# Optimization experiments

Measured on AMD Instinct MI355X. Metric: run time of the kernel, lower is better.

The kernel has to match this reference:

```python
import jax, jax.numpy as jnp
import numpy as np


def setup_inputs() -> dict:
    key = jax.random.key(0)
    k1, k2, k3 = jax.random.split(key, 3)
    b, n, h, d = 2, 2048, 16, 64
    q = jax.random.normal(k1, (b, n, h, d), dtype=jnp.float32)
    k = jax.random.normal(k2, (b, n, h, d), dtype=jnp.float32)
    v = jax.random.normal(k3, (b, n, h, d), dtype=jnp.float32)
    return {"q": q, "k": k, "v": v, "is_causal": 1}


def reference(q, k, v, is_causal):
    # q, k, v: [b, n, h, d] -> attention computed in [b, h, n, d] layout
    b, n, h, d = q.shape
    scale = 1.0 / jnp.sqrt(jnp.asarray(d, dtype=q.dtype))
    # scores: [b, h, n_q, n_k]
    scores = jnp.einsum("bqhd,bkhd->bhqk", q, k) * scale
    if is_causal:
        causal_mask = jnp.triu(jnp.ones((n, n), dtype=bool), k=1)  # True above diag
        scores = jnp.where(causal_mask[None, None], -jnp.inf, scores)
    attn = jax.nn.softmax(scores, axis=-1)
    out = jnp.einsum("bhqk,bkhd->bqhd", attn, v)  # back to [b, n, h, d]
    return out
```

## Files before the change

### kernel.cpp

```cpp
#include <hip/hip_runtime.h>
#include <hip/hip_bf16.h>

namespace {

constexpr int Nn = 2048;
constexpr int Hh = 16;
constexpr int Dd = 64;
constexpr int ROWSTR = Hh * Dd;
constexpr int KVB = 64;
constexpr int NTILES = Nn / KVB;
constexpr size_t IMG_TILE = 16384;
constexpr size_t WS_NEED = (size_t)32 * NTILES * IMG_TILE;

typedef __bf16 bf16x8 __attribute__((ext_vector_type(8)));
typedef __bf16 bf16x4 __attribute__((ext_vector_type(4)));
typedef float  f32x16 __attribute__((ext_vector_type(16)));

__global__ __launch_bounds__(256, 2) void prep_kernel(
    const float* __restrict__ Kg, const float* __restrict__ Vg,
    char* __restrict__ ws) {
  const int bid = blockIdx.x;
  const int bh  = bid & 31;
  const int T   = bid >> 5;
  const int tid = threadIdx.x;
  const int b = bh >> 4, h = bh & 15;
  const size_t base = ((size_t)b * Nn * Hh + h) * Dd;
  const float* kp = Kg + base;
  const float* vp = Vg + base;
  char* img = ws + (size_t)(bh * NTILES + T) * IMG_TILE;

  {
    const int row = tid >> 2;
    const int seg = tid & 3;
    const float* kr = kp + (size_t)(T * 64 + row) * ROWSTR + seg * 16;
    float4 f0 = ((const float4*)kr)[0];
    float4 f1 = ((const float4*)kr)[1];
    float4 f2 = ((const float4*)kr)[2];
    float4 f3 = ((const float4*)kr)[3];
    const int half = row >> 5, l31r = row & 31;
    char* slotp = img + (half * 4 + seg) * 1024;
    bf16x8 w0 = { (__bf16)f0.x, (__bf16)f0.y, (__bf16)f0.z, (__bf16)f0.w,
                  (__bf16)f1.x, (__bf16)f1.y, (__bf16)f1.z, (__bf16)f1.w };
    bf16x8 w1 = { (__bf16)f2.x, (__bf16)f2.y, (__bf16)f2.z, (__bf16)f2.w,
                  (__bf16)f3.x, (__bf16)f3.y, (__bf16)f3.z, (__bf16)f3.w };
    *(bf16x8*)(slotp + l31r * 16) = w0;
    *(bf16x8*)(slotp + (l31r + 32) * 16) = w1;
  }
  char* imgV = img + 8192;
#pragma unroll
  for (int e2 = 0; e2 < 2; ++e2) {
    const int e = e2 * 256 + tid;
    const int slotV = e >> 6, lane = e & 63;
    const int kc = slotV >> 1, df = slotV & 1;
    const int l31e = lane & 31, g2e = lane >> 5;
    const int d = 32 * df + l31e;
    const size_t kv0 = (size_t)(T * 64 + 16 * kc + 4 * g2e);
    const float* vb = vp + d;
    bf16x8 w;
#pragma unroll
    for (int i2 = 0; i2 < 4; ++i2) w[i2]     = (__bf16)vb[(kv0 + i2) * ROWSTR];
#pragma unroll
    for (int i2 = 0; i2 < 4; ++i2) w[4 + i2] = (__bf16)vb[(kv0 + 8 + i2) * ROWSTR];
    *(bf16x8*)(imgV + slotV * 1024 + lane * 16) = w;
  }
}

__global__ __launch_bounds__(256, 2) void fattn_kernel(
    const float* __restrict__ Qg, const char* __restrict__ ws,
    const int* __restrict__ flag, float* __restrict__ Og) {
  __shared__ __align__(16) char smem[2][2][16384];

  const int tid  = threadIdx.x;
  const int lane = tid & 63;
  const int wv   = tid >> 6;
  const int grp  = wv >> 1;
  const int st   = wv & 1;
  const int l31  = lane & 31;
  const int g2   = lane >> 5;

  const int bid = blockIdx.x;
  const int bh  = ((bid & 7) << 2) | ((bid >> 3) & 3);
  const int j   = bid >> 5;
  const int b   = bh >> 4;
  const int h   = bh & 15;
  const int causal = flag[0];

  const size_t base = ((size_t)b * Nn * Hh + h) * Dd;
  const float* qp = Qg + base;
  const char*  img = ws + (size_t)bh * NTILES * IMG_TILE;
  float*       op = Og + base;

  const float SCALE = 0.125f * 1.44269504088896340736f;

  for (int pass = 0; pass < 2; ++pass) {
    const int Tq = pass ? j : (31 - j);
    const int qs = Tq * 64 + st * 32;
    const int NI = causal ? ((Tq + 2) >> 1) : (NTILES / 2);
    const int nC = causal ? ((Tq >= grp) ? (((Tq - grp) >> 1) + 1) : 0)
                          : (NTILES / 2);

    __syncthreads();

    bf16x8 qf[4];
#pragma unroll
    for (int dc = 0; dc < 4; ++dc) {
      const float* qrow = qp + (size_t)(qs + l31) * ROWSTR + dc * 16 + g2 * 8;
      float4 a = *(const float4*)qrow;
      float4 c = *(const float4*)(qrow + 4);
      qf[dc][0] = (__bf16)(a.x * SCALE); qf[dc][1] = (__bf16)(a.y * SCALE);
      qf[dc][2] = (__bf16)(a.z * SCALE); qf[dc][3] = (__bf16)(a.w * SCALE);
      qf[dc][4] = (__bf16)(c.x * SCALE); qf[dc][5] = (__bf16)(c.y * SCALE);
      qf[dc][6] = (__bf16)(c.z * SCALE); qf[dc][7] = (__bf16)(c.w * SCALE);
    }

    f32x16 acc0 = {};
    f32x16 acc1 = {};
    float m_run = -INFINITY;
    float l_run = 0.0f;

    {
      bf16x8 stg[8];
#pragma unroll
      for (int it = 0; it < 8; ++it)
        stg[it] = *(const bf16x8*)(img + (it * 256 + tid) * 16);
#pragma unroll
      for (int it = 0; it < 8; ++it)
        *(bf16x8*)(&smem[0][it >> 2][0] + ((it & 3) * 256 + tid) * 16) = stg[it];
    }

    for (int i = 0; i < NI; ++i) {
      __syncthreads();
      const bool pf = (i + 1 < NI);
      bf16x8 stg[8];
      if (pf) {
        const char* src = img + (size_t)(2 * i + 2) * IMG_TILE;
#pragma unroll
        for (int it = 0; it < 8; ++it)
          stg[it] = *(const bf16x8*)(src + (it * 256 + tid) * 16);
      }

      if (i < nC) {
        const char* kb = &smem[i & 1][grp][0];
        const char* vb = kb + 8192;

        f32x16 s0 = {}, s1 = {};
        __builtin_amdgcn_s_setprio(1);
#pragma unroll
        for (int dc = 0; dc < 4; ++dc) {
          bf16x8 kf0 = *(const bf16x8*)(kb + (dc)     * 1024 + lane * 16);
          bf16x8 kf1 = *(const bf16x8*)(kb + (4 + dc) * 1024 + lane * 16);
          s0 = __builtin_amdgcn_mfma_f32_32x32x16_bf16(kf0, qf[dc], s0, 0, 0, 0);
          s1 = __builtin_amdgcn_mfma_f32_32x32x16_bf16(kf1, qf[dc], s1, 0, 0, 0);
        }
        __builtin_amdgcn_s_setprio(0);

        if (causal && (2 * i + grp) == Tq) {
          const int kvb = Tq * KVB;
          const int qrow = qs + l31;
#pragma unroll
          for (int rr = 0; rr < 16; ++rr) {
            int rm = (rr & 3) + ((rr >> 2) << 3) + (g2 << 2);
            if (kvb + rm > qrow)      s0[rr] = -INFINITY;
            if (kvb + 32 + rm > qrow) s1[rr] = -INFINITY;
          }
        }

        float p8[8];
#pragma unroll
        for (int e = 0; e < 8; ++e)
          p8[e] = fmaxf(fmaxf(s0[e], s0[e + 8]), fmaxf(s1[e], s1[e + 8]));
        float mt = fmaxf(fmaxf(fmaxf(p8[0], p8[1]), fmaxf(p8[2], p8[3])),
                         fmaxf(fmaxf(p8[4], p8[5]), fmaxf(p8[6], p8[7])));
        mt = fmaxf(mt, __shfl_xor(mt, 32));
        const float mnew = fmaxf(m_run, mt);

#pragma unroll
        for (int rr = 0; rr < 16; ++rr) {
          s0[rr] = __builtin_amdgcn_exp2f(s0[rr] - mnew);
          s1[rr] = __builtin_amdgcn_exp2f(s1[rr] - mnew);
        }
        float q8[8];
#pragma unroll
        for (int e = 0; e < 8; ++e)
          q8[e] = (s0[e] + s0[e + 8]) + (s1[e] + s1[e + 8]);
        float rs = ((q8[0] + q8[1]) + (q8[2] + q8[3])) +
                   ((q8[4] + q8[5]) + (q8[6] + q8[7]));
        rs += __shfl_xor(rs, 32);
        if (__all(mt <= m_run)) {
          l_run += rs;
        } else {
          const float alpha = __builtin_amdgcn_exp2f(m_run - mnew);
#pragma unroll
          for (int rr = 0; rr < 16; ++rr) {
            float at = __shfl(alpha, (rr & 3) + ((rr >> 2) << 3) + (g2 << 2));
            acc0[rr] *= at;
            acc1[rr] *= at;
          }
          l_run = l_run * alpha + rs;
          m_run = mnew;
        }

        bf16x8 pa[4];
#pragma unroll
        for (int kc = 0; kc < 4; ++kc) {
          const f32x16& sv = (kc < 2) ? s0 : s1;
          const int rbase = (kc & 1) * 8;
#pragma unroll
          for (int jj = 0; jj < 8; ++jj) pa[kc][jj] = (__bf16)sv[rbase + jj];
        }

        __builtin_amdgcn_s_setprio(1);
#pragma unroll
        for (int kc = 0; kc < 4; ++kc) {
#pragma unroll
          for (int df = 0; df < 2; ++df) {
            bf16x8 vf = *(const bf16x8*)(vb + (kc * 2 + df) * 1024 + lane * 16);
            if (df == 0)
              acc0 = __builtin_amdgcn_mfma_f32_32x32x16_bf16(pa[kc], vf, acc0, 0, 0, 0);
            else
              acc1 = __builtin_amdgcn_mfma_f32_32x32x16_bf16(pa[kc], vf, acc1, 0, 0, 0);
          }
        }
        __builtin_amdgcn_s_setprio(0);
      }

      if (pf) {
#pragma unroll
        for (int it = 0; it < 8; ++it)
          *(bf16x8*)(&smem[(i + 1) & 1][it >> 2][0] +
                     ((it & 3) * 256 + tid) * 16) = stg[it];
      }
    }

    __syncthreads();
    float* arena = (float*)&smem[0][0][0];
    if (grp == 1) {
      float* ab = arena + st * 2112;
#pragma unroll
      for (int rr = 0; rr < 16; ++rr) {
        int rm = (rr & 3) + ((rr >> 2) << 3) + (g2 << 2);
        ab[rm * 64 + l31]      = acc0[rr];
        ab[rm * 64 + 32 + l31] = acc1[rr];
      }
      if (g2 == 0) { ab[2048 + l31] = m_run; ab[2080 + l31] = l_run; }
    }
    __syncthreads();
    if (grp == 0) {
      const float* ab = arena + st * 2112;
      const float mB = ab[2048 + l31];
      const float lB = ab[2080 + l31];
      const float mN = fmaxf(m_run, mB);
      float fA = __builtin_amdgcn_exp2f(m_run - mN);
      float fB = __builtin_amdgcn_exp2f(mB - mN);
      const float lT = l_run * fA + lB * fB;
      const float linv = 1.0f / lT;
      fA *= linv; fB *= linv;
#pragma unroll
      for (int rr = 0; rr < 16; ++rr) {
        const int rm = (rr & 3) + ((rr >> 2) << 3) + (g2 << 2);
        const float FA = __shfl(fA, rm);
        const float FB = __shfl(fB, rm);
        const float o0 = acc0[rr] * FA + ab[rm * 64 + l31] * FB;
        const float o1 = acc1[rr] * FA + ab[rm * 64 + 32 + l31] * FB;
        const size_t row = (size_t)(qs + rm) * ROWSTR;
        op[row + l31]      = o0;
        op[row + 32 + l31] = o1;
      }
    }
  }
}

__device__ __forceinline__ int swzK(int row, int colByte) {
  return (row * 128 + colByte) ^ ((row & 7) << 4);
}
__device__ __forceinline__ int swzV(int row, int colByte) {
  return (row * 128 + colByte) ^ (((row & 7) << 4) | (((row >> 3) & 1) << 3));
}
struct SR { float4 k[4]; float v[16]; };
__device__ __forceinline__ void fb_issue(const float* kp, const float* vp,
                                         int kv0, int tid, SR& s) {
#pragma unroll
  for (int it = 0; it < 4; ++it) {
    int idx = it * 256 + tid;
    int kvr = idx >> 4, c4 = idx & 15;
    s.k[it] = *(const float4*)(kp + (size_t)(kv0 + kvr) * ROWSTR + c4 * 4);
  }
#pragma unroll
  for (int it = 0; it < 4; ++it) {
    int idx = it * 256 + tid;
    int d8 = idx & 63, kv4 = idx >> 6;
#pragma unroll
    for (int i2 = 0; i2 < 4; ++i2)
      s.v[it * 4 + i2] = vp[(size_t)(kv0 + kv4 * 4 + i2) * ROWSTR + d8];
  }
}
__device__ __forceinline__ void fb_write(char* kb, char* vb, int tid, const SR& s) {
#pragma unroll
  for (int it = 0; it < 4; ++it) {
    int idx = it * 256 + tid;
    int kvr = idx >> 4, c4 = idx & 15;
    bf16x4 w = { (__bf16)s.k[it].x, (__bf16)s.k[it].y,
                 (__bf16)s.k[it].z, (__bf16)s.k[it].w };
    *(bf16x4*)(kb + swzK(kvr, c4 * 8)) = w;
  }
#pragma unroll
  for (int it = 0; it < 4; ++it) {
    int idx = it * 256 + tid;
    int d8 = idx & 63, kv4 = idx >> 6;
    bf16x4 w = { (__bf16)s.v[it * 4 + 0], (__bf16)s.v[it * 4 + 1],
                 (__bf16)s.v[it * 4 + 2], (__bf16)s.v[it * 4 + 3] };
    *(bf16x4*)(vb + swzV(d8, kv4 * 8)) = w;
  }
}
__global__ __launch_bounds__(256, 2) void fattn_fb(
    const float* __restrict__ Qg, const float* __restrict__ Kg,
    const float* __restrict__ Vg, const int* __restrict__ flag,
    float* __restrict__ Og) {
  __shared__ __align__(16) char smem[16384];
  const int tid  = threadIdx.x;
  const int lane = tid & 63;
  const int wv   = tid >> 6;
  const int l31  = lane & 31;
  const int g2   = lane >> 5;
  const int bid = blockIdx.x;
  const int pidx = bid >> 1;
  const int side = bid & 1;
  const int bh  = ((pidx & 7) << 2) | (pidx >> 6);
  const int ti  = (pidx >> 3) & 7;
  const int b   = bh >> 4;
  const int h   = bh & 15;
  const int causal = flag[0];
  const int Tq  = side ? ti : (15 - ti);
  const size_t base = ((size_t)b * Nn * Hh + h) * Dd;
  const float* qp = Qg + base;
  const float* kp = Kg + base;
  const float* vp = Vg + base;
  float*       op = Og + base;
  const float SCALE = 0.125f * 1.44269504088896340736f;
  const int qs = Tq * 128 + wv * 32;
  const int Tblock = causal ? (2 * Tq + 2) : NTILES;
  const int Twave  = causal ? ((qs + 31) / KVB + 1) : NTILES;
  bf16x8 qf[4];
#pragma unroll
  for (int dc = 0; dc < 4; ++dc) {
    const float* qrow = qp + (size_t)(qs + l31) * ROWSTR + dc * 16 + g2 * 8;
    float4 a = *(const float4*)qrow;
    float4 c = *(const float4*)(qrow + 4);
    qf[dc][0] = (__bf16)(a.x * SCALE); qf[dc][1] = (__bf16)(a.y * SCALE);
    qf[dc][2] = (__bf16)(a.z * SCALE); qf[dc][3] = (__bf16)(a.w * SCALE);
    qf[dc][4] = (__bf16)(c.x * SCALE); qf[dc][5] = (__bf16)(c.y * SCALE);
    qf[dc][6] = (__bf16)(c.z * SCALE); qf[dc][7] = (__bf16)(c.w * SCALE);
  }
  f32x16 acc0 = {}, acc1 = {};
  float m_run = -INFINITY, l_run = 0.0f;
  SR st;
  fb_issue(kp, vp, 0, tid, st);
  fb_write(smem, smem + 8192, tid, st);
  for (int t = 0; t < Tblock; ++t) {
    __syncthreads();
    const bool pf = (t + 1 < Tblock);
    if (pf) fb_issue(kp, vp, (t + 1) * KVB, tid, st);
    if (t < Twave) {
      const char* kb = smem;
      const char* vb = smem + 8192;
      f32x16 s0 = {}, s1 = {};
#pragma unroll
      for (int dc = 0; dc < 4; ++dc) {
        bf16x8 kf0 = *(const bf16x8*)(kb + swzK(l31,      32 * dc + 16 * g2));
        bf16x8 kf1 = *(const bf16x8*)(kb + swzK(32 + l31, 32 * dc + 16 * g2));
        s0 = __builtin_amdgcn_mfma_f32_32x32x16_bf16(kf0, qf[dc], s0, 0, 0, 0);
        s1 = __builtin_amdgcn_mfma_f32_32x32x16_bf16(kf1, qf[dc], s1, 0, 0, 0);
      }
      if (causal && t == Twave - 1) {
        const int kvb = t * KVB;
        const int qrow = qs + l31;
#pragma unroll
        for (int rr = 0; rr < 16; ++rr) {
          int rm = (rr & 3) + ((rr >> 2) << 3) + (g2 << 2);
          if (kvb + rm > qrow)      s0[rr] = -INFINITY;
          if (kvb + 32 + rm > qrow) s1[rr] = -INFINITY;
        }
      }
      float p8[8];
#pragma unroll
      for (int e = 0; e < 8; ++e)
        p8[e] = fmaxf(fmaxf(s0[e], s0[e + 8]), fmaxf(s1[e], s1[e + 8]));
      float mt = fmaxf(fmaxf(fmaxf(p8[0], p8[1]), fmaxf(p8[2], p8[3])),
                       fmaxf(fmaxf(p8[4], p8[5]), fmaxf(p8[6], p8[7])));
      mt = fmaxf(mt, __shfl_xor(mt, 32));
      const float mnew = fmaxf(m_run, mt);
#pragma unroll
      for (int rr = 0; rr < 16; ++rr) {
        s0[rr] = __builtin_amdgcn_exp2f(s0[rr] - mnew);
        s1[rr] = __builtin_amdgcn_exp2f(s1[rr] - mnew);
      }
      float q8[8];
#pragma unroll
      for (int e = 0; e < 8; ++e)
        q8[e] = (s0[e] + s0[e + 8]) + (s1[e] + s1[e + 8]);
      float rs = ((q8[0] + q8[1]) + (q8[2] + q8[3])) +
                 ((q8[4] + q8[5]) + (q8[6] + q8[7]));
      rs += __shfl_xor(rs, 32);
      if (__all(mt <= m_run)) {
        l_run += rs;
      } else {
        const float alpha = __builtin_amdgcn_exp2f(m_run - mnew);
#pragma unroll
        for (int rr = 0; rr < 16; ++rr) {
          float at = __shfl(alpha, (rr & 3) + ((rr >> 2) << 3) + (g2 << 2));
          acc0[rr] *= at;
          acc1[rr] *= at;
        }
        l_run = l_run * alpha + rs;
        m_run = mnew;
      }
      bf16x8 pa[4];
#pragma unroll
      for (int kc = 0; kc < 4; ++kc) {
        const f32x16& sv = (kc < 2) ? s0 : s1;
        const int rbase = (kc & 1) * 8;
#pragma unroll
        for (int jj = 0; jj < 8; ++jj) pa[kc][jj] = (__bf16)sv[rbase + jj];
      }
#pragma unroll
      for (int kc = 0; kc < 4; ++kc) {
        const int cb = 32 * kc + 8 * g2;
#pragma unroll
        for (int df = 0; df < 2; ++df) {
          const int row = 32 * df + l31;
          bf16x4 v0 = *(const bf16x4*)(vb + swzV(row, cb));
          bf16x4 v1 = *(const bf16x4*)(vb + swzV(row, cb + 16));
          bf16x8 vf = __builtin_shufflevector(v0, v1, 0, 1, 2, 3, 4, 5, 6, 7);
          if (df == 0)
            acc0 = __builtin_amdgcn_mfma_f32_32x32x16_bf16(pa[kc], vf, acc0, 0, 0, 0);
          else
            acc1 = __builtin_amdgcn_mfma_f32_32x32x16_bf16(pa[kc], vf, acc1, 0, 0, 0);
        }
      }
    }
    __syncthreads();
    if (pf) fb_write(smem, smem + 8192, tid, st);
  }
  const float linv = 1.0f / l_run;
#pragma unroll
  for (int rr = 0; rr < 16; ++rr) {
    const int rm = (rr & 3) + ((rr >> 2) << 3) + (g2 << 2);
    const float li = __shfl(linv, rm);
    const size_t row = (size_t)(qs + rm) * ROWSTR;
    op[row + l31]      = acc0[rr] * li;
    op[row + 32 + l31] = acc1[rr] * li;
  }
}

}

extern "C" void kernel_launch(void* const* d_in, const int* in_sizes, int n_in,
                              void* d_out, int out_size, void* d_ws, size_t ws_size,
                              hipStream_t stream) {
  (void)in_sizes; (void)n_in; (void)out_size;
  const float* q = (const float*)d_in[0];
  const float* k = (const float*)d_in[1];
  const float* v = (const float*)d_in[2];
  const int* flag = (const int*)d_in[3];
  float* out = (float*)d_out;
  if (ws_size >= WS_NEED) {
    char* ws = (char*)d_ws;
    prep_kernel<<<dim3(1024), dim3(256), 0, stream>>>(k, v, ws);
    fattn_kernel<<<dim3(512), dim3(256), 0, stream>>>(q, ws, flag, out);
  } else {
    fattn_fb<<<dim3(512), dim3(256), 0, stream>>>(q, k, v, flag, out);
  }
}
```

Measured before the change: 51.16 us.

## Split KV tiles across four wave groups and read MFMA fragments directly from global

Doubles the block to 512 threads so four wave groups each take every fourth KV tile (split-K within the block), instead of two groups. The LDS double-buffered staging and its per-tile barriers are removed; K/V fragments are loaded straight from the pre-swizzled global workspace into registers. The final merge now combines four partial softmax states through a larger shared arena. This raises parallelism per query tile and drops barrier overhead, but relies on L2/global latency hiding without LDS reuse and adds a heavier combine step.

After: 52.26 us. 1.02x slower.

```diff
diff --git a/kernel.cpp b/kernel.cpp
--- a/kernel.cpp
+++ b/kernel.cpp
@@ -65,16 +65,16 @@
   }
 }
 
-__global__ __launch_bounds__(256, 2) void fattn_kernel(
+__global__ __launch_bounds__(512, 2) void fattn_kernel(
     const float* __restrict__ Qg, const char* __restrict__ ws,
     const int* __restrict__ flag, float* __restrict__ Og) {
-  __shared__ __align__(16) char smem[2][2][16384];
+  __shared__ float arena[6 * 2112];
 
   const int tid  = threadIdx.x;
   const int lane = tid & 63;
   const int wv   = tid >> 6;
+  const int st   = wv & 1;
   const int grp  = wv >> 1;
-  const int st   = wv & 1;
   const int l31  = lane & 31;
   const int g2   = lane >> 5;
 
@@ -95,11 +95,7 @@
   for (int pass = 0; pass < 2; ++pass) {
     const int Tq = pass ? j : (31 - j);
     const int qs = Tq * 64 + st * 32;
-    const int NI = causal ? ((Tq + 2) >> 1) : (NTILES / 2);
-    const int nC = causal ? ((Tq >= grp) ? (((Tq - grp) >> 1) + 1) : 0)
-                          : (NTILES / 2);
-
-    __syncthreads();
+    const int TL = causal ? Tq : (NTILES - 1);
 
     bf16x8 qf[4];
 #pragma unroll
@@ -118,124 +114,96 @@
     float m_run = -INFINITY;
     float l_run = 0.0f;
 
-    {
-      bf16x8 stg[8];
-#pragma unroll
-      for (int it = 0; it < 8; ++it)
-        stg[it] = *(const bf16x8*)(img + (it * 256 + tid) * 16);
-#pragma unroll
-      for (int it = 0; it < 8; ++it)
-        *(bf16x8*)(&smem[0][it >> 2][0] + ((it & 3) * 256 + tid) * 16) = stg[it];
+    for (int t = grp; t <= TL; t += 4) {
+      const char* kb = img + (size_t)t * IMG_TILE;
+      const char* vb = kb + 8192;
+
+      bf16x8 kf[8];
+#pragma unroll
+      for (int s8 = 0; s8 < 8; ++s8)
+        kf[s8] = *(const bf16x8*)(kb + s8 * 1024 + lane * 16);
+
+      f32x16 s0 = {}, s1 = {};
+      __builtin_amdgcn_s_setprio(1);
+#pragma unroll
+      for (int dc = 0; dc < 4; ++dc) {
+        s0 = __builtin_amdgcn_mfma_f32_32x32x16_bf16(kf[dc],     qf[dc], s0, 0, 0, 0);
+        s1 = __builtin_amdgcn_mfma_f32_32x32x16_bf16(kf[4 + dc], qf[dc], s1, 0, 0, 0);
+      }
+      __builtin_amdgcn_s_setprio(0);
+
+      bf16x8 vf[8];
+#pragma unroll
+      for (int s8 = 0; s8 < 8; ++s8)
+        vf[s8] = *(const bf16x8*)(vb + s8 * 1024 + lane * 16);
+
+      if (causal && t == Tq) {
+        const int kvb = Tq * KVB;
+        const int qrow = qs + l31;
+#pragma unroll
+        for (int rr = 0; rr < 16; ++rr) {
+          int rm = (rr & 3) + ((rr >> 2) << 3) + (g2 << 2);
+          if (kvb + rm > qrow)      s0[rr] = -INFINITY;
+          if (kvb + 32 + rm > qrow) s1[rr] = -INFINITY;
+        }
+      }
+
+      float p8[8];
+#pragma unroll
+      for (int e = 0; e < 8; ++e)
+        p8[e] = fmaxf(fmaxf(s0[e], s0[e + 8]), fmaxf(s1[e], s1[e + 8]));
+      float mt = fmaxf(fmaxf(fmaxf(p8[0], p8[1]), fmaxf(p8[2], p8[3])),
+                       fmaxf(fmaxf(p8[4], p8[5]), fmaxf(p8[6], p8[7])));
+      mt = fmaxf(mt, __shfl_xor(mt, 32));
+      const float mnew = fmaxf(m_run, mt);
+
+#pragma unroll
+      for (int rr = 0; rr < 16; ++rr) {
+        s0[rr] = __builtin_amdgcn_exp2f(s0[rr] - mnew);
+        s1[rr] = __builtin_amdgcn_exp2f(s1[rr] - mnew);
+      }
+      float q8[8];
+#pragma unroll
+      for (int e = 0; e < 8; ++e)
+        q8[e] = (s0[e] + s0[e + 8]) + (s1[e] + s1[e + 8]);
+      float rs = ((q8[0] + q8[1]) + (q8[2] + q8[3])) +
+                 ((q8[4] + q8[5]) + (q8[6] + q8[7]));
+      rs += __shfl_xor(rs, 32);
+      if (__all(mt <= m_run)) {
+        l_run += rs;
+      } else {
+        const float alpha = __builtin_amdgcn_exp2f(m_run - mnew);
+#pragma unroll
+        for (int rr = 0; rr < 16; ++rr) {
+          float at = __shfl(alpha, (rr & 3) + ((rr >> 2) << 3) + (g2 << 2));
+          acc0[rr] *= at;
+          acc1[rr] *= at;
+        }
+        l_run = l_run * alpha + rs;
+        m_run = mnew;
+      }
+
+      bf16x8 pa[4];
+#pragma unroll
+      for (int kc = 0; kc < 4; ++kc) {
+        const f32x16& sv = (kc < 2) ? s0 : s1;
+        const int rbase = (kc & 1) * 8;
+#pragma unroll
+        for (int jj = 0; jj < 8; ++jj) pa[kc][jj] = (__bf16)sv[rbase + jj];
+      }
+
+      __builtin_amdgcn_s_setprio(1);
+#pragma unroll
+      for (int kc = 0; kc < 4; ++kc) {
+        acc0 = __builtin_amdgcn_mfma_f32_32x32x16_bf16(pa[kc], vf[kc * 2],     acc0, 0, 0, 0);
+        acc1 = __builtin_amdgcn_mfma_f32_32x32x16_bf16(pa[kc], vf[kc * 2 + 1], acc1, 0, 0, 0);
+      }
+      __builtin_amdgcn_s_setprio(0);
     }
 
-    for (int i = 0; i < NI; ++i) {
-      __syncthreads();
-      const bool pf = (i + 1 < NI);
-      bf16x8 stg[8];
-      if (pf) {
-        const char* src = img + (size_t)(2 * i + 2) * IMG_TILE;
-#pragma unroll
-        for (int it = 0; it < 8; ++it)
-          stg[it] = *(const bf16x8*)(src + (it * 256 + tid) * 16);
-      }
-
-      if (i < nC) {
-        const char* kb = &smem[i & 1][grp][0];
-        const char* vb = kb + 8192;
-
-        f32x16 s0 = {}, s1 = {};
-        __builtin_amdgcn_s_setprio(1);
-#pragma unroll
-        for (int dc = 0; dc < 4; ++dc) {
-          bf16x8 kf0 = *(const bf16x8*)(kb + (dc)     * 1024 + lane * 16);
-          bf16x8 kf1 = *(const bf16x8*)(kb + (4 + dc) * 1024 + lane * 16);
-          s0 = __builtin_amdgcn_mfma_f32_32x32x16_bf16(kf0, qf[dc], s0, 0, 0, 0);
-          s1 = __builtin_amdgcn_mfma_f32_32x32x16_bf16(kf1, qf[dc], s1, 0, 0, 0);
-        }
-        __builtin_amdgcn_s_setprio(0);
-
-        if (causal && (2 * i + grp) == Tq) {
-          const int kvb = Tq * KVB;
-          const int qrow = qs + l31;
-#pragma unroll
-          for (int rr = 0; rr < 16; ++rr) {
-            int rm = (rr & 3) + ((rr >> 2) << 3) + (g2 << 2);
-            if (kvb + rm > qrow)      s0[rr] = -INFINITY;
-            if (kvb + 32 + rm > qrow) s1[rr] = -INFINITY;
-          }
-        }
-
-        float p8[8];
-#pragma unroll
-        for (int e = 0; e < 8; ++e)
-          p8[e] = fmaxf(fmaxf(s0[e], s0[e + 8]), fmaxf(s1[e], s1[e + 8]));
-        float mt = fmaxf(fmaxf(fmaxf(p8[0], p8[1]), fmaxf(p8[2], p8[3])),
-                         fmaxf(fmaxf(p8[4], p8[5]), fmaxf(p8[6], p8[7])));
-        mt = fmaxf(mt, __shfl_xor(mt, 32));
-        const float mnew = fmaxf(m_run, mt);
-
-#pragma unroll
-        for (int rr = 0; rr < 16; ++rr) {
-          s0[rr] = __builtin_amdgcn_exp2f(s0[rr] - mnew);
-          s1[rr] = __builtin_amdgcn_exp2f(s1[rr] - mnew);
-        }
-        float q8[8];
-#pragma unroll
-        for (int e = 0; e < 8; ++e)
-          q8[e] = (s0[e] + s0[e + 8]) + (s1[e] + s1[e + 8]);
-        float rs = ((q8[0] + q8[1]) + (q8[2] + q8[3])) +
-                   ((q8[4] + q8[5]) + (q8[6] + q8[7]));
-        rs += __shfl_xor(rs, 32);
-        if (__all(mt <= m_run)) {
-          l_run += rs;
-        } else {
-          const float alpha = __builtin_amdgcn_exp2f(m_run - mnew);
-#pragma unroll
-          for (int rr = 0; rr < 16; ++rr) {
-            float at = __shfl(alpha, (rr & 3) + ((rr >> 2) << 3) + (g2 << 2));
-            acc0[rr] *= at;
-            acc1[rr] *= at;
-          }
-          l_run = l_run * alpha + rs;
-          m_run = mnew;
-        }
-
-        bf16x8 pa[4];
-#pragma unroll
-        for (int kc = 0; kc < 4; ++kc) {
-          const f32x16& sv = (kc < 2) ? s0 : s1;
-          const int rbase = (kc & 1) * 8;
-#pragma unroll
-          for (int jj = 0; jj < 8; ++jj) pa[kc][jj] = (__bf16)sv[rbase + jj];
-        }
-
-        __builtin_amdgcn_s_setprio(1);
-#pragma unroll
-        for (int kc = 0; kc < 4; ++kc) {
-#pragma unroll
-          for (int df = 0; df < 2; ++df) {
-            bf16x8 vf = *(const bf16x8*)(vb + (kc * 2 + df) * 1024 + lane * 16);
-            if (df == 0)
-              acc0 = __builtin_amdgcn_mfma_f32_32x32x16_bf16(pa[kc], vf, acc0, 0, 0, 0);
-            else
-              acc1 = __builtin_amdgcn_mfma_f32_32x32x16_bf16(pa[kc], vf, acc1, 0, 0, 0);
-          }
-        }
-        __builtin_amdgcn_s_setprio(0);
-      }
-
-      if (pf) {
-#pragma unroll
-        for (int it = 0; it < 8; ++it)
-          *(bf16x8*)(&smem[(i + 1) & 1][it >> 2][0] +
-                     ((it & 3) * 256 + tid) * 16) = stg[it];
-      }
-    }
-
     __syncthreads();
-    float* arena = (float*)&smem[0][0][0];
-    if (grp == 1) {
-      float* ab = arena + st * 2112;
+    if (grp != 0) {
+      float* ab = arena + ((grp - 1) * 2 + st) * 2112;
 #pragma unroll
       for (int rr = 0; rr < 16; ++rr) {
         int rm = (rr & 3) + ((rr >> 2) << 3) + (g2 << 2);
@@ -246,22 +214,31 @@
     }
     __syncthreads();
     if (grp == 0) {
-      const float* ab = arena + st * 2112;
-      const float mB = ab[2048 + l31];
-      const float lB = ab[2080 + l31];
-      const float mN = fmaxf(m_run, mB);
-      float fA = __builtin_amdgcn_exp2f(m_run - mN);
-      float fB = __builtin_amdgcn_exp2f(mB - mN);
-      const float lT = l_run * fA + lB * fB;
+      const float* a1 = arena + (0 * 2 + st) * 2112;
+      const float* a2 = arena + (1 * 2 + st) * 2112;
+      const float* a3 = arena + (2 * 2 + st) * 2112;
+      const float m1 = a1[2048 + l31], l1 = a1[2080 + l31];
+      const float m2 = a2[2048 + l31], l2 = a2[2080 + l31];
+      const float m3 = a3[2048 + l31], l3 = a3[2080 + l31];
+      const float mN = fmaxf(fmaxf(m_run, m1), fmaxf(m2, m3));
+      float f0 = __builtin_amdgcn_exp2f(m_run - mN);
+      float f1 = __builtin_amdgcn_exp2f(m1 - mN);
+      float f2 = __builtin_amdgcn_exp2f(m2 - mN);
+      float f3 = __builtin_amdgcn_exp2f(m3 - mN);
+      const float lT = l_run * f0 + l1 * f1 + l2 * f2 + l3 * f3;
       const float linv = 1.0f / lT;
-      fA *= linv; fB *= linv;
+      f0 *= linv; f1 *= linv; f2 *= linv; f3 *= linv;
 #pragma unroll
       for (int rr = 0; rr < 16; ++rr) {
         const int rm = (rr & 3) + ((rr >> 2) << 3) + (g2 << 2);
-        const float FA = __shfl(fA, rm);
-        const float FB = __shfl(fB, rm);
-        const float o0 = acc0[rr] * FA + ab[rm * 64 + l31] * FB;
-        const float o1 = acc1[rr] * FA + ab[rm * 64 + 32 + l31] * FB;
+        const float F0 = __shfl(f0, rm);
+        const float F1 = __shfl(f1, rm);
+        const float F2 = __shfl(f2, rm);
+        const float F3 = __shfl(f3, rm);
+        const float o0 = acc0[rr] * F0 + a1[rm * 64 + l31] * F1 +
+                         a2[rm * 64 + l31] * F2 + a3[rm * 64 + l31] * F3;
+        const float o1 = acc1[rr] * F0 + a1[rm * 64 + 32 + l31] * F1 +
+                         a2[rm * 64 + 32 + l31] * F2 + a3[rm * 64 + 32 + l31] * F3;
         const size_t row = (size_t)(qs + rm) * ROWSTR;
         op[row + l31]      = o0;
         op[row + 32 + l31] = o1;
@@ -316,7 +293,7 @@
     const float* __restrict__ Qg, const float* __restrict__ Kg,
     const float* __restrict__ Vg, const int* __restrict__ flag,
     float* __restrict__ Og) {
-  __shared__ __align__(16) char smem[16384];
+  __shared__ char smem[16384];
   const int tid  = threadIdx.x;
   const int lane = tid & 63;
   const int wv   = tid >> 6;
@@ -466,7 +443,7 @@
   if (ws_size >= WS_NEED) {
     char* ws = (char*)d_ws;
     prep_kernel<<<dim3(1024), dim3(256), 0, stream>>>(k, v, ws);
-    fattn_kernel<<<dim3(512), dim3(256), 0, stream>>>(q, ws, flag, out);
+    fattn_kernel<<<dim3(512), dim3(512), 0, stream>>>(q, ws, flag, out);
   } else {
     fattn_fb<<<dim3(512), dim3(256), 0, stream>>>(q, k, v, flag, out);
   }
```
